# Kernel tuning notes

Measured on AMD Instinct MI355X. Metric: run time of the kernel, lower is better.

## Reference

```python
import jax, jax.numpy as jnp
import numpy as np

K = 3
STRIDE = 1
PAD = 1
EPS = 1e-5


def conv2d(x, w, b):
    # x [B,C,H,W], w [O,I,K,K], b [O]
    y = jax.lax.conv_general_dilated(
        x, w, (STRIDE, STRIDE), [(PAD, PAD), (PAD, PAD)],
        dimension_numbers=("NCHW", "OIHW", "NCHW"))
    return y + b[None, :, None, None]


def _bilinear_sample(img, py, px):
    # img [C,H,W]; py,px [KK,Ho,Wo] continuous coords; zero outside bounds
    H, W = img.shape[1], img.shape[2]
    y0 = jnp.floor(py)
    x0 = jnp.floor(px)
    wy1 = py - y0
    wx1 = px - x0
    wy0 = 1.0 - wy1
    wx0 = 1.0 - wx1

    def gather(yi, xi):
        valid = (yi >= 0) & (yi < H) & (xi >= 0) & (xi < W)
        yc = jnp.clip(yi, 0, H - 1).astype(jnp.int32)
        xc = jnp.clip(xi, 0, W - 1).astype(jnp.int32)
        v = img[:, yc, xc]  # [C,KK,Ho,Wo]
        return v * valid.astype(img.dtype)[None]

    out = (gather(y0, x0) * (wy0 * wx0)[None]
           + gather(y0, x0 + 1) * (wy0 * wx1)[None]
           + gather(y0 + 1, x0) * (wy1 * wx0)[None]
           + gather(y0 + 1, x0 + 1) * (wy1 * wx1)[None])
    return out  # [C,KK,Ho,Wo]


def deform_conv_bn_act(x, w_off, b_off, w_mod, b_mod, w_dc, gamma, beta):
    B, C, H, W = x.shape
    Cout = w_dc.shape[0]
    KK = K * K
    Ho = (H + 2 * PAD - K) // STRIDE + 1
    Wo = (W + 2 * PAD - K) // STRIDE + 1

    offset = conv2d(x, w_off, b_off)                 # [B,2*KK,Ho,Wo]
    modulation = jax.nn.sigmoid(conv2d(x, w_mod, b_mod))  # [B,KK,Ho,Wo]

    off = offset.reshape(B, KK, 2, Ho, Wo)
    dy, dx = off[:, :, 0], off[:, :, 1]              # [B,KK,Ho,Wo]

    ky = jnp.repeat(jnp.arange(K), K).astype(x.dtype)   # kernel row index per tap
    kx = jnp.tile(jnp.arange(K), K).astype(x.dtype)     # kernel col index per tap
    base_y = (jnp.arange(Ho, dtype=x.dtype) * STRIDE - PAD)[None, :, None] + ky[:, None, None]
    base_x = (jnp.arange(Wo, dtype=x.dtype) * STRIDE - PAD)[None, None, :] + kx[:, None, None]
    py = dy + base_y[None]                           # [B,KK,Ho,Wo]
    px = dx + base_x[None]

    sampled = jax.vmap(_bilinear_sample)(x, py, px)  # [B,C,KK,Ho,Wo]
    sampled = sampled * modulation[:, None]          # modulation per tap

    out = jnp.einsum("bckhw,ock->bohw", sampled, w_dc.reshape(Cout, C, KK))

    # BatchNorm (training-mode batch statistics, biased variance)
    mean = jnp.mean(out, axis=(0, 2, 3), keepdims=True)
    var = jnp.mean((out - mean) ** 2, axis=(0, 2, 3), keepdims=True)
    out = (out - mean) * jax.lax.rsqrt(var + EPS)
    out = out * gamma[None, :, None, None] + beta[None, :, None, None]

    return jax.nn.silu(out)


def setup_inputs() -> dict:
    key = jax.random.key(0)
    ks = jax.random.split(key, 8)
    B, Cin, Cout, H, W = 8, 128, 256, 64, 64
    x = jax.random.normal(ks[0], (B, Cin, H, W), dtype=jnp.float32)
    # small random offset/modulation weights (the literal init is all-zero, which
    # would make the deform conv degenerate to a plain conv)
    w_off = jax.random.normal(ks[1], (2 * K * K, Cin, K, K), dtype=jnp.float32) * 0.01
    b_off = jnp.zeros((2 * K * K,), dtype=jnp.float32)
    w_mod = jax.random.normal(ks[2], (K * K, Cin, K, K), dtype=jnp.float32) * 0.01
    b_mod = jnp.ones((K * K,), dtype=jnp.float32)
    fan_in = Cin * K * K
    w_dc = jax.random.normal(ks[3], (Cout, Cin, K, K), dtype=jnp.float32) / np.sqrt(fan_in)
    gamma = 1.0 + 0.1 * jax.random.normal(ks[4], (Cout,), dtype=jnp.float32)
    beta = 0.1 * jax.random.normal(ks[5], (Cout,), dtype=jnp.float32)
    return {"x": x, "w_off": w_off, "b_off": b_off, "w_mod": w_mod,
            "b_mod": b_mod, "w_dc": w_dc, "gamma": gamma, "beta": beta}


def reference(x, w_off, b_off, w_mod, b_mod, w_dc, gamma, beta):
    return deform_conv_bn_act(x, w_off, b_off, w_mod, b_mod, w_dc, gamma, beta)
```

## Files before the change

kernel.cpp:

```cpp
#include <hip/hip_runtime.h>
#include <hip/hip_bf16.h>
#include <math.h>

#define H_ 64
#define W_ 64
#define CIN 128
#define COUT 256
#define NB 8
#define KK9 9
#define NPIX 4096
#define KTOT 1152
#define NCK 36
#define KPAD 40

typedef short short8_t __attribute__((ext_vector_type(8)));
typedef float floatx4 __attribute__((ext_vector_type(4)));

__device__ __forceinline__ unsigned short f2bf(float f) {
    union { float f; unsigned u; } v; v.f = f;
    unsigned r = v.u + 0x7FFF + ((v.u >> 16) & 1);
    return (unsigned short)(r >> 16);
}
__device__ __forceinline__ float bf2f(unsigned short h) {
    union { unsigned u; float f; } v; v.u = ((unsigned)h) << 16;
    return v.f;
}

#if defined(__has_builtin)
#if __has_builtin(__builtin_amdgcn_global_load_lds)
#define HAVE_GLOAD_LDS 1
#endif
#endif

#ifdef HAVE_GLOAD_LDS
__device__ __forceinline__ void gload_lds16(const unsigned int* g, unsigned int* l) {
    __builtin_amdgcn_global_load_lds(
        (const __attribute__((address_space(1))) unsigned int*)g,
        (__attribute__((address_space(3))) unsigned int*)l, 16, 0, 0);
}
#endif

__global__ __launch_bounds__(256) void k_offmod(
    const float* __restrict__ x, const float* __restrict__ w_off,
    const float* __restrict__ b_off, const float* __restrict__ w_mod,
    const float* __restrict__ b_mod, float* __restrict__ ppy,
    float* __restrict__ ppx, float* __restrict__ pmod)
{
    __shared__ float xp[16][10][12];
    __shared__ float wb[27][16][12];
    const int t = threadIdx.x;
    const int tx = blockIdx.x, ty = blockIdx.y, b = blockIdx.z;
    const int q = t & 15, g = t >> 4;
    const int lpy = q >> 1, lpx4 = (q & 1) * 4;
    float acc[2][4] = {};

    for (int cc = 0; cc < CIN; cc += 16) {
        __syncthreads();
        for (int idx = t; idx < 1600; idx += 256) {
            int c = idx / 100, r = (idx % 100) / 10, col = idx % 10;
            int gy = ty * 8 - 1 + r, gx = tx * 8 - 1 + col;
            float v = 0.f;
            if (gy >= 0 && gy < H_ && gx >= 0 && gx < W_)
                v = x[((b * CIN + cc + c) * H_ + gy) * W_ + gx];
            xp[c][r][col] = v;
        }
        for (int idx = t; idx < 27 * 16 * 9; idx += 256) {
            int ch = idx / 144, rr = idx % 144, c = rr / 9, tap = rr % 9;
            wb[ch][c][tap] = (ch < 18)
                ? w_off[(ch * CIN + cc + c) * 9 + tap]
                : w_mod[((ch - 18) * CIN + cc + c) * 9 + tap];
        }
        __syncthreads();

        for (int c = 0; c < 16; ++c) {
            float xv[3][8];
            #pragma unroll
            for (int ky = 0; ky < 3; ++ky) {
                float4 v0 = *(const float4*)&xp[c][lpy + ky][lpx4];
                float4 v1 = *(const float4*)&xp[c][lpy + ky][lpx4 + 4];
                xv[ky][0] = v0.x; xv[ky][1] = v0.y; xv[ky][2] = v0.z; xv[ky][3] = v0.w;
                xv[ky][4] = v1.x; xv[ky][5] = v1.y; xv[ky][6] = v1.z; xv[ky][7] = v1.w;
            }
            #pragma unroll
            for (int i = 0; i < 2; ++i) {
                int ch = g + 16 * i;
                if (ch < 27) {
                    const float* wr = &wb[ch][c][0];
                    #pragma unroll
                    for (int ky = 0; ky < 3; ++ky)
                        #pragma unroll
                        for (int kx = 0; kx < 3; ++kx) {
                            float wv = wr[ky * 3 + kx];
                            #pragma unroll
                            for (int p = 0; p < 4; ++p)
                                acc[i][p] += xv[ky][p + kx] * wv;
                        }
                }
            }
        }
    }

    const int ho = ty * 8 + lpy;
    #pragma unroll
    for (int i = 0; i < 2; ++i) {
        int ch = g + 16 * i;
        if (ch >= 27) continue;
        #pragma unroll
        for (int p = 0; p < 4; ++p) {
            int wo = tx * 8 + lpx4 + p;
            int pix = ho * W_ + wo;
            if (ch < 18) {
                float v = acc[i][p] + b_off[ch];
                int kk = ch >> 1;
                if ((ch & 1) == 0)
                    ppy[(b * KK9 + kk) * NPIX + pix] = v + (float)(ho - 1 + kk / 3);
                else
                    ppx[(b * KK9 + kk) * NPIX + pix] = v + (float)(wo - 1 + kk % 3);
            } else {
                int km = ch - 18;
                float v = acc[i][p] + b_mod[km];
                pmod[(b * KK9 + km) * NPIX + pix] = 1.f / (1.f + expf(-v));
            }
        }
    }
}

__global__ __launch_bounds__(256) void k_prep(
    const float* __restrict__ w_dc, unsigned short* __restrict__ wsplit)
{
    int idx = blockIdx.x * 256 + threadIdx.x;
    int kl = idx % KPAD;
    int rest = idx / KPAD;
    int o = rest & 255;
    int rest2 = rest >> 8;
    int hl = rest2 & 1, ck = rest2 >> 1;
    unsigned short v = 0;
    if (kl < 32) {
        int kp = ck * 32 + kl;
        int kk = kp >> 7, c = kp & 127;
        float w = w_dc[o * KTOT + c * 9 + kk];
        unsigned short hi = f2bf(w);
        v = hl ? f2bf(w - bf2f(hi)) : hi;
    }
    wsplit[idx] = v;
}

__global__ __launch_bounds__(256, 2) void k_main(
    const float* __restrict__ x, const unsigned short* __restrict__ wsplit,
    const float* __restrict__ ppy, const float* __restrict__ ppx,
    const float* __restrict__ pmod, float* __restrict__ out,
    float* __restrict__ gsum, float* __restrict__ gsq)
{
    __shared__ __align__(16) unsigned short Wsp[2 * COUT * KPAD];
    __shared__ __align__(16) unsigned short Ssp[2 * 64 * KPAD];
    __shared__ float ppl[3][KK9][64];
    __shared__ float redS[COUT], redQ[COUT];

    const int t = threadIdx.x;
    const int b = blockIdx.x & 7;
    const int pix0 = (blockIdx.x >> 3) * 64;
    const int lane = t & 63, wm = t >> 6;

    for (int idx = t; idx < 3 * KK9 * 64; idx += 256) {
        int arr = idx / (KK9 * 64), rem = idx - arr * (KK9 * 64);
        int kk = rem >> 6, p = rem & 63;
        const float* src = (arr == 0) ? ppy : (arr == 1) ? ppx : pmod;
        ppl[arr][kk][p] = src[(b * KK9 + kk) * NPIX + pix0 + p];
    }
    __syncthreads();

    floatx4 acc[4][4] = {};
    const float* xb = x + b * CIN * NPIX;
    const int pxl = t & 63, kg = t >> 6;
    const int o_lane = lane & 15, g4 = lane >> 4;

    for (int kk = 0; kk < KK9; ++kk) {
        float py = ppl[0][kk][pxl];
        float px = ppl[1][kk][pxl];
        float m  = ppl[2][kk][pxl];
        float y0f = floorf(py), x0f = floorf(px);
        float wy1 = py - y0f, wx1 = px - x0f;
        float wy0 = 1.f - wy1, wx0 = 1.f - wx1;
        int y0 = (int)y0f, x0 = (int)x0f;
        bool y0v = (unsigned)y0 < (unsigned)H_;
        bool y1v = (unsigned)(y0 + 1) < (unsigned)H_;
        bool x0v = (unsigned)x0 < (unsigned)W_;
        bool x1v = (unsigned)(x0 + 1) < (unsigned)W_;
        float w00 = (y0v && x0v) ? wy0 * wx0 * m : 0.f;
        float w01 = (y0v && x1v) ? wy0 * wx1 * m : 0.f;
        float w10 = (y1v && x0v) ? wy1 * wx0 * m : 0.f;
        float w11 = (y1v && x1v) ? wy1 * wx1 * m : 0.f;
        int y0c = min(max(y0, 0), H_ - 1), y1c = min(max(y0 + 1, 0), H_ - 1);
        int x0c = min(max(x0, 0), W_ - 1), x1c = min(max(x0 + 1, 0), W_ - 1);
        int a00 = y0c * W_ + x0c, a01 = y0c * W_ + x1c;
        int a10 = y1c * W_ + x0c, a11 = y1c * W_ + x1c;

        for (int sub = 0; sub < 4; ++sub) {
            const int ck = kk * 4 + sub;
            __syncthreads();
            {
                const unsigned short* wsrc = wsplit + ck * (2 * COUT * KPAD);
#ifdef HAVE_GLOAD_LDS
                #pragma unroll
                for (int i = 0; i < 10; ++i) {
                    int slice = i * 4 + wm;
                    gload_lds16((const unsigned int*)(wsrc + slice * 512 + lane * 8),
                                (unsigned int*)(Wsp + slice * 512));
                }
#else
                const float4* s4 = (const float4*)wsrc;
                float4* d4 = (float4*)Wsp;
                #pragma unroll
                for (int i = 0; i < 10; ++i)
                    d4[i * 256 + t] = s4[i * 256 + t];
#endif
            }
            {
                const int c0 = sub * 32 + kg * 8;
                const float* pl = xb + c0 * NPIX;
                unsigned short hs[8], ls[8];
                #pragma unroll
                for (int j = 0; j < 8; ++j) {
                    float s = pl[a00] * w00 + pl[a01] * w01 +
                              pl[a10] * w10 + pl[a11] * w11;
                    union { float f; unsigned u; } su; su.f = s;
                    hs[j] = (unsigned short)(su.u >> 16);
                    union { unsigned u; float f; } hf; hf.u = su.u & 0xFFFF0000u;
                    union { float f; unsigned u; } du; du.f = s - hf.f;
                    ls[j] = (unsigned short)(du.u >> 16);
                    pl += NPIX;
                }
                union { unsigned short u[8]; short8_t v; } ph, plo;
                #pragma unroll
                for (int j = 0; j < 8; ++j) { ph.u[j] = hs[j]; plo.u[j] = ls[j]; }
                *(short8_t*)(Ssp + pxl * KPAD + kg * 8) = ph.v;
                *(short8_t*)(Ssp + 64 * KPAD + pxl * KPAD + kg * 8) = plo.v;
            }
            __syncthreads();

            short8_t bh[4], bl[4];
            #pragma unroll
            for (int ni = 0; ni < 4; ++ni) {
                int pxf = ni * 16 + o_lane;
                bh[ni] = *(const short8_t*)(Ssp + pxf * KPAD + g4 * 8);
                bl[ni] = *(const short8_t*)(Ssp + 64 * KPAD + pxf * KPAD + g4 * 8);
            }
            #pragma unroll
            for (int mi = 0; mi < 4; ++mi) {
                int of = wm * 64 + mi * 16 + o_lane;
                short8_t ah = *(const short8_t*)(Wsp + of * KPAD + g4 * 8);
                short8_t al = *(const short8_t*)(Wsp + COUT * KPAD + of * KPAD + g4 * 8);
                #pragma unroll
                for (int ni = 0; ni < 4; ++ni) {
                    acc[mi][ni] = __builtin_amdgcn_mfma_f32_16x16x32_bf16(
                        ah, bh[ni], acc[mi][ni], 0, 0, 0);
                    acc[mi][ni] = __builtin_amdgcn_mfma_f32_16x16x32_bf16(
                        ah, bl[ni], acc[mi][ni], 0, 0, 0);
                    acc[mi][ni] = __builtin_amdgcn_mfma_f32_16x16x32_bf16(
                        al, bh[ni], acc[mi][ni], 0, 0, 0);
                }
            }
        }
    }

    #pragma unroll
    for (int mi = 0; mi < 4; ++mi) {
        #pragma unroll
        for (int r = 0; r < 4; ++r) {
            float s = 0.f, q = 0.f;
            #pragma unroll
            for (int ni = 0; ni < 4; ++ni) {
                float v = acc[mi][ni][r];
                s += v; q += v * v;
            }
            s += __shfl_xor(s, 1); q += __shfl_xor(q, 1);
            s += __shfl_xor(s, 2); q += __shfl_xor(q, 2);
            s += __shfl_xor(s, 4); q += __shfl_xor(q, 4);
            s += __shfl_xor(s, 8); q += __shfl_xor(q, 8);
            if (o_lane == 0) {
                int o = wm * 64 + mi * 16 + g4 * 4 + r;
                redS[o] = s;
                redQ[o] = q;
            }
        }
    }
    __syncthreads();
    if (t < COUT) {
        atomicAdd(&gsum[t], redS[t]);
        atomicAdd(&gsq[t],  redQ[t]);
    }

    #pragma unroll
    for (int mi = 0; mi < 4; ++mi) {
        int o_base = wm * 64 + mi * 16 + g4 * 4;
        #pragma unroll
        for (int ni = 0; ni < 4; ++ni) {
            int px = pix0 + ni * 16 + o_lane;
            #pragma unroll
            for (int r = 0; r < 4; ++r)
                out[(b * COUT + o_base + r) * NPIX + px] = acc[mi][ni][r];
        }
    }
}

__global__ __launch_bounds__(256) void k_bnact(
    float* __restrict__ out, const float* __restrict__ gsum,
    const float* __restrict__ gsq, const float* __restrict__ gamma,
    const float* __restrict__ beta)
{
    int idx = blockIdx.x * 256 + threadIdx.x;
    int o = (idx >> 10) & 255;
    const float invn = 1.f / 32768.f;
    float mean = gsum[o] * invn;
    float var = gsq[o] * invn - mean * mean;
    float scale = gamma[o] * rsqrtf(var + 1e-5f);
    float shift = beta[o] - mean * scale;
    float4* p = (float4*)out;
    float4 v = p[idx];
    float y;
    y = v.x * scale + shift; v.x = y / (1.f + expf(-y));
    y = v.y * scale + shift; v.y = y / (1.f + expf(-y));
    y = v.z * scale + shift; v.z = y / (1.f + expf(-y));
    y = v.w * scale + shift; v.w = y / (1.f + expf(-y));
    p[idx] = v;
}

extern "C" void kernel_launch(void* const* d_in, const int* in_sizes, int n_in,
                              void* d_out, int out_size, void* d_ws, size_t ws_size,
                              hipStream_t stream)
{
    (void)in_sizes; (void)n_in; (void)out_size; (void)ws_size;
    const float* x     = (const float*)d_in[0];
    const float* w_off = (const float*)d_in[1];
    const float* b_off = (const float*)d_in[2];
    const float* w_mod = (const float*)d_in[3];
    const float* b_mod = (const float*)d_in[4];
    const float* w_dc  = (const float*)d_in[5];
    const float* gamma = (const float*)d_in[6];
    const float* beta  = (const float*)d_in[7];
    float* out = (float*)d_out;
    float* ws  = (float*)d_ws;

    const int NPK = NB * KK9 * NPIX;
    float* ppy  = ws;
    float* ppx  = ws + NPK;
    float* pmod = ws + 2 * NPK;
    unsigned short* wsplit = (unsigned short*)(ws + 3 * NPK);
    float* gsum = ws + 3 * NPK + 368640;
    float* gsq  = gsum + 256;

    hipMemsetAsync(gsum, 0, 512 * sizeof(float), stream);
    hipLaunchKernelGGL(k_offmod, dim3(8, 8, NB), dim3(256), 0, stream,
                       x, w_off, b_off, w_mod, b_mod, ppy, ppx, pmod);
    hipLaunchKernelGGL(k_prep, dim3(2880), dim3(256), 0, stream,
                       w_dc, wsplit);
    hipLaunchKernelGGL(k_main, dim3(512), dim3(256), 0, stream,
                       x, wsplit, ppy, ppx, pmod, out, gsum, gsq);
    hipLaunchKernelGGL(k_bnact, dim3(8192), dim3(256), 0, stream,
                       out, gsum, gsq, gamma, beta);
}
```

Measured before the change: 332.4 us.

## Move offset conv to MFMA and double-buffer main gather with register weights

Replaces the scalar FP32 offset/modulation conv with an implicit-GEMM kernel on bf16 MFMA, using hi/lo split weights and double-buffered LDS. The main deform kernel stops staging weights through LDS and reads A fragments straight from global memory. It also prefetches the next chunk's bilinear gathers into registers during the current MFMA batch, ping-pongs the LDS sample buffer, and does the BN statistics atomics straight from the shuffles. The offset conv rounds only the activations to a single bf16 term, so predicted offsets can differ slightly from the reference. The offset kernel launches just 128 blocks, which risks underusing the GPU.

```diff
diff --git a/kernel.cpp b/kernel.cpp
--- a/kernel.cpp
+++ b/kernel.cpp
@@ -11,7 +11,8 @@
 #define NPIX 4096
 #define KTOT 1152
 #define NCK 36
-#define KPAD 40
+#define SPAD 40
+#define OSP 40
 
 typedef short short8_t __attribute__((ext_vector_type(8)));
 typedef float floatx4 __attribute__((ext_vector_type(4)));
@@ -26,144 +27,157 @@
     return v.f;
 }
 
-#if defined(__has_builtin)
-#if __has_builtin(__builtin_amdgcn_global_load_lds)
-#define HAVE_GLOAD_LDS 1
-#endif
-#endif
-
-#ifdef HAVE_GLOAD_LDS
-__device__ __forceinline__ void gload_lds16(const unsigned int* g, unsigned int* l) {
-    __builtin_amdgcn_global_load_lds(
-        (const __attribute__((address_space(1))) unsigned int*)g,
-        (__attribute__((address_space(3))) unsigned int*)l, 16, 0, 0);
-}
-#endif
-
-__global__ __launch_bounds__(256) void k_offmod(
-    const float* __restrict__ x, const float* __restrict__ w_off,
-    const float* __restrict__ b_off, const float* __restrict__ w_mod,
-    const float* __restrict__ b_mod, float* __restrict__ ppy,
-    float* __restrict__ ppx, float* __restrict__ pmod)
-{
-    __shared__ float xp[16][10][12];
-    __shared__ float wb[27][16][12];
+__global__ __launch_bounds__(256) void k_prep_dc(
+    const float* __restrict__ w_dc, unsigned short* __restrict__ wsplit)
+{
+    int idx = blockIdx.x * 256 + threadIdx.x;
+    int kl = idx & 31;
+    int o  = (idx >> 5) & 255;
+    int rest = idx >> 13;
+    int hl = rest & 1, ck = rest >> 1;
+    int kp = ck * 32 + kl;
+    int kk = kp >> 7, c = kp & 127;
+    float w = w_dc[o * KTOT + c * 9 + kk];
+    unsigned short hi = f2bf(w);
+    wsplit[idx] = hl ? f2bf(w - bf2f(hi)) : hi;
+}
+
+__global__ __launch_bounds__(256) void k_prep_om(
+    const float* __restrict__ w_off, const float* __restrict__ w_mod,
+    unsigned short* __restrict__ womsplit)
+{
+    int idx = blockIdx.x * 256 + threadIdx.x;
+    int kl = idx & 31;
+    int o  = (idx >> 5) & 31;
+    int rest = idx >> 10;
+    int hl = rest & 1, ck = rest >> 1;
+    int kp = ck * 32 + kl;
+    int kk = kp >> 7, c = kp & 127;
+    float w = 0.f;
+    if (o < 18)      w = w_off[(o * CIN + c) * 9 + kk];
+    else if (o < 27) w = w_mod[((o - 18) * CIN + c) * 9 + kk];
+    unsigned short hi = f2bf(w);
+    womsplit[idx] = hl ? f2bf(w - bf2f(hi)) : hi;
+}
+
+__global__ __launch_bounds__(256, 4) void k_off2(
+    const float* __restrict__ x, const unsigned short* __restrict__ womsplit,
+    const float* __restrict__ b_off, const float* __restrict__ b_mod,
+    float* __restrict__ ppy, float* __restrict__ ppx, float* __restrict__ pmod)
+{
+    __shared__ __align__(16) unsigned short S2[2][256 * OSP];
+
     const int t = threadIdx.x;
-    const int tx = blockIdx.x, ty = blockIdx.y, b = blockIdx.z;
-    const int q = t & 15, g = t >> 4;
-    const int lpy = q >> 1, lpx4 = (q & 1) * 4;
-    float acc[2][4] = {};
-
-    for (int cc = 0; cc < CIN; cc += 16) {
+    const int b = blockIdx.x & 7;
+    const int pix0 = (blockIdx.x >> 3) * 256;
+    const int lane = t & 63, wid = t >> 6;
+    const int o_lane = lane & 15, g4 = lane >> 4;
+
+    const float* xb = x + b * CIN * NPIX;
+    const int pix = pix0 + t;
+    const int ho = pix >> 6, wo2 = pix & 63;
+
+    floatx4 acc[2][4] = {};
+    float g[32];
+    int addr = 0; float wmask = 0.f;
+
+    auto SETUP2 = [&](int kkv) {
+        int sy = ho + (kkv / 3) - 1, sx = wo2 + (kkv % 3) - 1;
+        bool v = ((unsigned)sy < (unsigned)H_) && ((unsigned)sx < (unsigned)W_);
+        wmask = v ? 1.f : 0.f;
+        addr = min(max(sy, 0), H_ - 1) * W_ + min(max(sx, 0), W_ - 1);
+    };
+    auto GATH2 = [&](int ck) {
+        const float* pl = xb + ((ck & 3) * 32) * NPIX + addr;
+        #pragma unroll
+        for (int j = 0; j < 32; ++j) { g[j] = pl[0]; pl += NPIX; }
+    };
+    auto WR2 = [&](int buf) {
+        #pragma unroll
+        for (int q = 0; q < 4; ++q) {
+            union { unsigned short u[8]; short8_t v; } p;
+            #pragma unroll
+            for (int j = 0; j < 8; ++j) p.u[j] = f2bf(g[q * 8 + j] * wmask);
+            *(short8_t*)(&S2[buf][t * OSP + q * 8]) = p.v;
+        }
+    };
+
+    SETUP2(0); GATH2(0); WR2(0);
+    __syncthreads();
+
+    for (int tt = 0; tt < NCK; ++tt) {
+        short8_t ah[2], al[2];
+        #pragma unroll
+        for (int mi = 0; mi < 2; ++mi) {
+            const unsigned short* wb_ =
+                womsplit + ((tt * 2 + 0) * 32 + mi * 16 + o_lane) * 32 + g4 * 8;
+            ah[mi] = *(const short8_t*)wb_;
+            al[mi] = *(const short8_t*)(wb_ + 1024);
+        }
+        if (tt + 1 < NCK) { SETUP2((tt + 1) >> 2); GATH2(tt + 1); }
+        #pragma unroll
+        for (int ni = 0; ni < 4; ++ni) {
+            int pxf = wid * 64 + ni * 16 + o_lane;
+            short8_t bb = *(const short8_t*)(&S2[tt & 1][pxf * OSP + g4 * 8]);
+            #pragma unroll
+            for (int mi = 0; mi < 2; ++mi) {
+                acc[mi][ni] = __builtin_amdgcn_mfma_f32_16x16x32_bf16(
+                    ah[mi], bb, acc[mi][ni], 0, 0, 0);
+                acc[mi][ni] = __builtin_amdgcn_mfma_f32_16x16x32_bf16(
+                    al[mi], bb, acc[mi][ni], 0, 0, 0);
+            }
+        }
+        if (tt + 1 < NCK) WR2((tt + 1) & 1);
         __syncthreads();
-        for (int idx = t; idx < 1600; idx += 256) {
-            int c = idx / 100, r = (idx % 100) / 10, col = idx % 10;
-            int gy = ty * 8 - 1 + r, gx = tx * 8 - 1 + col;
-            float v = 0.f;
-            if (gy >= 0 && gy < H_ && gx >= 0 && gx < W_)
-                v = x[((b * CIN + cc + c) * H_ + gy) * W_ + gx];
-            xp[c][r][col] = v;
-        }
-        for (int idx = t; idx < 27 * 16 * 9; idx += 256) {
-            int ch = idx / 144, rr = idx % 144, c = rr / 9, tap = rr % 9;
-            wb[ch][c][tap] = (ch < 18)
-                ? w_off[(ch * CIN + cc + c) * 9 + tap]
-                : w_mod[((ch - 18) * CIN + cc + c) * 9 + tap];
-        }
-        __syncthreads();
-
-        for (int c = 0; c < 16; ++c) {
-            float xv[3][8];
-            #pragma unroll
-            for (int ky = 0; ky < 3; ++ky) {
-                float4 v0 = *(const float4*)&xp[c][lpy + ky][lpx4];
-                float4 v1 = *(const float4*)&xp[c][lpy + ky][lpx4 + 4];
-                xv[ky][0] = v0.x; xv[ky][1] = v0.y; xv[ky][2] = v0.z; xv[ky][3] = v0.w;
-                xv[ky][4] = v1.x; xv[ky][5] = v1.y; xv[ky][6] = v1.z; xv[ky][7] = v1.w;
-            }
-            #pragma unroll
-            for (int i = 0; i < 2; ++i) {
-                int ch = g + 16 * i;
-                if (ch < 27) {
-                    const float* wr = &wb[ch][c][0];
-                    #pragma unroll
-                    for (int ky = 0; ky < 3; ++ky)
-                        #pragma unroll
-                        for (int kx = 0; kx < 3; ++kx) {
-                            float wv = wr[ky * 3 + kx];
-                            #pragma unroll
-                            for (int p = 0; p < 4; ++p)
-                                acc[i][p] += xv[ky][p + kx] * wv;
-                        }
+    }
+
+    #pragma unroll
+    for (int mi = 0; mi < 2; ++mi) {
+        #pragma unroll
+        for (int r = 0; r < 4; ++r) {
+            int o = mi * 16 + g4 * 4 + r;
+            if (o >= 27) continue;
+            #pragma unroll
+            for (int ni = 0; ni < 4; ++ni) {
+                int pp = pix0 + wid * 64 + ni * 16 + o_lane;
+                float v = acc[mi][ni][r];
+                int hoo = pp >> 6, woo = pp & 63;
+                if (o < 18) {
+                    int kk2 = o >> 1;
+                    float vv = v + b_off[o];
+                    if ((o & 1) == 0)
+                        ppy[(b * KK9 + kk2) * NPIX + pp] = vv + (float)(hoo - 1 + kk2 / 3);
+                    else
+                        ppx[(b * KK9 + kk2) * NPIX + pp] = vv + (float)(woo - 1 + kk2 % 3);
+                } else {
+                    int km = o - 18;
+                    float vv = v + b_mod[km];
+                    pmod[(b * KK9 + km) * NPIX + pp] = 1.f / (1.f + expf(-vv));
                 }
             }
         }
     }
-
-    const int ho = ty * 8 + lpy;
-    #pragma unroll
-    for (int i = 0; i < 2; ++i) {
-        int ch = g + 16 * i;
-        if (ch >= 27) continue;
-        #pragma unroll
-        for (int p = 0; p < 4; ++p) {
-            int wo = tx * 8 + lpx4 + p;
-            int pix = ho * W_ + wo;
-            if (ch < 18) {
-                float v = acc[i][p] + b_off[ch];
-                int kk = ch >> 1;
-                if ((ch & 1) == 0)
-                    ppy[(b * KK9 + kk) * NPIX + pix] = v + (float)(ho - 1 + kk / 3);
-                else
-                    ppx[(b * KK9 + kk) * NPIX + pix] = v + (float)(wo - 1 + kk % 3);
-            } else {
-                int km = ch - 18;
-                float v = acc[i][p] + b_mod[km];
-                pmod[(b * KK9 + km) * NPIX + pix] = 1.f / (1.f + expf(-v));
-            }
-        }
-    }
-}
-
-__global__ __launch_bounds__(256) void k_prep(
-    const float* __restrict__ w_dc, unsigned short* __restrict__ wsplit)
-{
-    int idx = blockIdx.x * 256 + threadIdx.x;
-    int kl = idx % KPAD;
-    int rest = idx / KPAD;
-    int o = rest & 255;
-    int rest2 = rest >> 8;
-    int hl = rest2 & 1, ck = rest2 >> 1;
-    unsigned short v = 0;
-    if (kl < 32) {
-        int kp = ck * 32 + kl;
-        int kk = kp >> 7, c = kp & 127;
-        float w = w_dc[o * KTOT + c * 9 + kk];
-        unsigned short hi = f2bf(w);
-        v = hl ? f2bf(w - bf2f(hi)) : hi;
-    }
-    wsplit[idx] = v;
-}
-
-__global__ __launch_bounds__(256, 2) void k_main(
+}
+
+__global__ __launch_bounds__(256, 3) void k_main(
     const float* __restrict__ x, const unsigned short* __restrict__ wsplit,
     const float* __restrict__ ppy, const float* __restrict__ ppx,
     const float* __restrict__ pmod, float* __restrict__ out,
     float* __restrict__ gsum, float* __restrict__ gsq)
 {
-    __shared__ __align__(16) unsigned short Wsp[2 * COUT * KPAD];
-    __shared__ __align__(16) unsigned short Ssp[2 * 64 * KPAD];
+    __shared__ __align__(16) unsigned short Ssp[2][2 * 64 * SPAD];
     __shared__ float ppl[3][KK9][64];
-    __shared__ float redS[COUT], redQ[COUT];
 
     const int t = threadIdx.x;
     const int b = blockIdx.x & 7;
     const int pix0 = (blockIdx.x >> 3) * 64;
-    const int lane = t & 63, wm = t >> 6;
+    const int lane = t & 63, wid = t >> 6;
+    const int o_lane = lane & 15, g4 = lane >> 4;
+    const int pxl = t & 63, kg = t >> 6;
 
     for (int idx = t; idx < 3 * KK9 * 64; idx += 256) {
-        int arr = idx / (KK9 * 64), rem = idx - arr * (KK9 * 64);
-        int kk = rem >> 6, p = rem & 63;
+        int arr = idx / (KK9 * 64), rem2 = idx - arr * (KK9 * 64);
+        int kk = rem2 >> 6, p = rem2 & 63;
         const float* src = (arr == 0) ? ppy : (arr == 1) ? ppx : pmod;
         ppl[arr][kk][p] = src[(b * KK9 + kk) * NPIX + pix0 + p];
     }
@@ -171,13 +185,15 @@
 
     floatx4 acc[4][4] = {};
     const float* xb = x + b * CIN * NPIX;
-    const int pxl = t & 63, kg = t >> 6;
-    const int o_lane = lane & 15, g4 = lane >> 4;
-
-    for (int kk = 0; kk < KK9; ++kk) {
-        float py = ppl[0][kk][pxl];
-        float px = ppl[1][kk][pxl];
-        float m  = ppl[2][kk][pxl];
+
+    float g00[8], g01[8], g10[8], g11[8];
+    float w00, w01, w10, w11;
+    int a00, a01, a10, a11;
+
+    auto SETUP = [&](int kkv) {
+        float py = ppl[0][kkv][pxl];
+        float px = ppl[1][kkv][pxl];
+        float m  = ppl[2][kkv][pxl];
         float y0f = floorf(py), x0f = floorf(px);
         float wy1 = py - y0f, wx1 = px - x0f;
         float wy0 = 1.f - wy1, wx0 = 1.f - wx1;
@@ -186,81 +202,69 @@
         bool y1v = (unsigned)(y0 + 1) < (unsigned)H_;
         bool x0v = (unsigned)x0 < (unsigned)W_;
         bool x1v = (unsigned)(x0 + 1) < (unsigned)W_;
-        float w00 = (y0v && x0v) ? wy0 * wx0 * m : 0.f;
-        float w01 = (y0v && x1v) ? wy0 * wx1 * m : 0.f;
-        float w10 = (y1v && x0v) ? wy1 * wx0 * m : 0.f;
-        float w11 = (y1v && x1v) ? wy1 * wx1 * m : 0.f;
+        w00 = (y0v && x0v) ? wy0 * wx0 * m : 0.f;
+        w01 = (y0v && x1v) ? wy0 * wx1 * m : 0.f;
+        w10 = (y1v && x0v) ? wy1 * wx0 * m : 0.f;
+        w11 = (y1v && x1v) ? wy1 * wx1 * m : 0.f;
         int y0c = min(max(y0, 0), H_ - 1), y1c = min(max(y0 + 1, 0), H_ - 1);
         int x0c = min(max(x0, 0), W_ - 1), x1c = min(max(x0 + 1, 0), W_ - 1);
-        int a00 = y0c * W_ + x0c, a01 = y0c * W_ + x1c;
-        int a10 = y1c * W_ + x0c, a11 = y1c * W_ + x1c;
-
-        for (int sub = 0; sub < 4; ++sub) {
-            const int ck = kk * 4 + sub;
-            __syncthreads();
-            {
-                const unsigned short* wsrc = wsplit + ck * (2 * COUT * KPAD);
-#ifdef HAVE_GLOAD_LDS
-                #pragma unroll
-                for (int i = 0; i < 10; ++i) {
-                    int slice = i * 4 + wm;
-                    gload_lds16((const unsigned int*)(wsrc + slice * 512 + lane * 8),
-                                (unsigned int*)(Wsp + slice * 512));
-                }
-#else
-                const float4* s4 = (const float4*)wsrc;
-                float4* d4 = (float4*)Wsp;
-                #pragma unroll
-                for (int i = 0; i < 10; ++i)
-                    d4[i * 256 + t] = s4[i * 256 + t];
-#endif
-            }
-            {
-                const int c0 = sub * 32 + kg * 8;
-                const float* pl = xb + c0 * NPIX;
-                unsigned short hs[8], ls[8];
-                #pragma unroll
-                for (int j = 0; j < 8; ++j) {
-                    float s = pl[a00] * w00 + pl[a01] * w01 +
-                              pl[a10] * w10 + pl[a11] * w11;
-                    union { float f; unsigned u; } su; su.f = s;
-                    hs[j] = (unsigned short)(su.u >> 16);
-                    union { unsigned u; float f; } hf; hf.u = su.u & 0xFFFF0000u;
-                    union { float f; unsigned u; } du; du.f = s - hf.f;
-                    ls[j] = (unsigned short)(du.u >> 16);
-                    pl += NPIX;
-                }
-                union { unsigned short u[8]; short8_t v; } ph, plo;
-                #pragma unroll
-                for (int j = 0; j < 8; ++j) { ph.u[j] = hs[j]; plo.u[j] = ls[j]; }
-                *(short8_t*)(Ssp + pxl * KPAD + kg * 8) = ph.v;
-                *(short8_t*)(Ssp + 64 * KPAD + pxl * KPAD + kg * 8) = plo.v;
-            }
-            __syncthreads();
-
-            short8_t bh[4], bl[4];
-            #pragma unroll
-            for (int ni = 0; ni < 4; ++ni) {
-                int pxf = ni * 16 + o_lane;
-                bh[ni] = *(const short8_t*)(Ssp + pxf * KPAD + g4 * 8);
-                bl[ni] = *(const short8_t*)(Ssp + 64 * KPAD + pxf * KPAD + g4 * 8);
-            }
+        a00 = y0c * W_ + x0c; a01 = y0c * W_ + x1c;
+        a10 = y1c * W_ + x0c; a11 = y1c * W_ + x1c;
+    };
+    auto GATHER = [&](int ck) {
+        const float* pl = xb + ((ck & 3) * 32 + kg * 8) * NPIX;
+        #pragma unroll
+        for (int j = 0; j < 8; ++j) {
+            g00[j] = pl[a00]; g01[j] = pl[a01];
+            g10[j] = pl[a10]; g11[j] = pl[a11];
+            pl += NPIX;
+        }
+    };
+    auto WRITES = [&](int buf) {
+        union { unsigned short u[8]; short8_t v; } ph, plo;
+        #pragma unroll
+        for (int j = 0; j < 8; ++j) {
+            float s = g00[j] * w00 + g01[j] * w01 + g10[j] * w10 + g11[j] * w11;
+            union { float f; unsigned u; } su; su.f = s;
+            ph.u[j] = (unsigned short)(su.u >> 16);
+            union { unsigned u; float f; } hf; hf.u = su.u & 0xFFFF0000u;
+            union { float f; unsigned u; } du; du.f = s - hf.f;
+            plo.u[j] = (unsigned short)(du.u >> 16);
+        }
+        *(short8_t*)(&Ssp[buf][pxl * SPAD + kg * 8]) = ph.v;
+        *(short8_t*)(&Ssp[buf][64 * SPAD + pxl * SPAD + kg * 8]) = plo.v;
+    };
+
+    SETUP(0); GATHER(0); WRITES(0);
+    __syncthreads();
+
+    for (int tt = 0; tt < NCK; ++tt) {
+        short8_t ah[4], al[4];
+        #pragma unroll
+        for (int mi = 0; mi < 4; ++mi) {
+            const unsigned short* wb_ =
+                wsplit + ((tt * 2 + 0) * 256 + wid * 64 + mi * 16 + o_lane) * 32 + g4 * 8;
+            ah[mi] = *(const short8_t*)wb_;
+            al[mi] = *(const short8_t*)(wb_ + 8192);
+        }
+        if (tt + 1 < NCK) { SETUP((tt + 1) >> 2); GATHER(tt + 1); }
+        #pragma unroll
+        for (int ni = 0; ni < 4; ++ni) {
+            int pxf = ni * 16 + o_lane;
+            short8_t bh = *(const short8_t*)(&Ssp[tt & 1][pxf * SPAD + g4 * 8]);
+            short8_t bl = *(const short8_t*)(&Ssp[tt & 1][64 * SPAD + pxf * SPAD + g4 * 8]);
             #pragma unroll
             for (int mi = 0; mi < 4; ++mi) {
-                int of = wm * 64 + mi * 16 + o_lane;
-                short8_t ah = *(const short8_t*)(Wsp + of * KPAD + g4 * 8);
-                short8_t al = *(const short8_t*)(Wsp + COUT * KPAD + of * KPAD + g4 * 8);
-                #pragma unroll
-                for (int ni = 0; ni < 4; ++ni) {
-                    acc[mi][ni] = __builtin_amdgcn_mfma_f32_16x16x32_bf16(
-                        ah, bh[ni], acc[mi][ni], 0, 0, 0);
-                    acc[mi][ni] = __builtin_amdgcn_mfma_f32_16x16x32_bf16(
-                        ah, bl[ni], acc[mi][ni], 0, 0, 0);
-                    acc[mi][ni] = __builtin_amdgcn_mfma_f32_16x16x32_bf16(
-                        al, bh[ni], acc[mi][ni], 0, 0, 0);
-                }
-            }
-        }
+                acc[mi][ni] = __builtin_amdgcn_mfma_f32_16x16x32_bf16(
+                    ah[mi], bh, acc[mi][ni], 0, 0, 0);
+                acc[mi][ni] = __builtin_amdgcn_mfma_f32_16x16x32_bf16(
+                    ah[mi], bl, acc[mi][ni], 0, 0, 0);
+                acc[mi][ni] = __builtin_amdgcn_mfma_f32_16x16x32_bf16(
+                    al[mi], bh, acc[mi][ni], 0, 0, 0);
+            }
+        }
+        if (tt + 1 < NCK) WRITES((tt + 1) & 1);
+        __syncthreads();
     }
 
     #pragma unroll
@@ -278,21 +282,16 @@
             s += __shfl_xor(s, 4); q += __shfl_xor(q, 4);
             s += __shfl_xor(s, 8); q += __shfl_xor(q, 8);
             if (o_lane == 0) {
-                int o = wm * 64 + mi * 16 + g4 * 4 + r;
-                redS[o] = s;
-                redQ[o] = q;
-            }
-        }
-    }
-    __syncthreads();
-    if (t < COUT) {
-        atomicAdd(&gsum[t], redS[t]);
-        atomicAdd(&gsq[t],  redQ[t]);
+                int o = wid * 64 + mi * 16 + g4 * 4 + r;
+                atomicAdd(&gsum[o], s);
+                atomicAdd(&gsq[o],  q);
+            }
+        }
     }
 
     #pragma unroll
     for (int mi = 0; mi < 4; ++mi) {
-        int o_base = wm * 64 + mi * 16 + g4 * 4;
+        int o_base = wid * 64 + mi * 16 + g4 * 4;
         #pragma unroll
         for (int ni = 0; ni < 4; ++ni) {
             int px = pix0 + ni * 16 + o_lane;
@@ -345,15 +344,17 @@
     float* ppy  = ws;
     float* ppx  = ws + NPK;
     float* pmod = ws + 2 * NPK;
-    unsigned short* wsplit = (unsigned short*)(ws + 3 * NPK);
-    float* gsum = ws + 3 * NPK + 368640;
+    unsigned short* wsplit   = (unsigned short*)(ws + 3 * NPK);
+    unsigned short* womsplit = (unsigned short*)(ws + 3 * NPK + 294912);
+    float* gsum = ws + 3 * NPK + 294912 + 36864;
     float* gsq  = gsum + 256;
 
     hipMemsetAsync(gsum, 0, 512 * sizeof(float), stream);
-    hipLaunchKernelGGL(k_offmod, dim3(8, 8, NB), dim3(256), 0, stream,
-                       x, w_off, b_off, w_mod, b_mod, ppy, ppx, pmod);
-    hipLaunchKernelGGL(k_prep, dim3(2880), dim3(256), 0, stream,
-                       w_dc, wsplit);
+    hipLaunchKernelGGL(k_prep_dc, dim3(2304), dim3(256), 0, stream, w_dc, wsplit);
+    hipLaunchKernelGGL(k_prep_om, dim3(288), dim3(256), 0, stream,
+                       w_off, w_mod, womsplit);
+    hipLaunchKernelGGL(k_off2, dim3(128), dim3(256), 0, stream,
+                       x, womsplit, b_off, b_mod, ppy, ppx, pmod);
     hipLaunchKernelGGL(k_main, dim3(512), dim3(256), 0, stream,
                        x, wsplit, ppy, ppx, pmod, out, gsum, gsq);
     hipLaunchKernelGGL(k_bnact, dim3(8192), dim3(256), 0, stream,
```

New measurement: 290.3 us. 1.15x faster.
